# Optimization experiments

Hardware: AMD Instinct MI355X
Metric: run time of the kernel (lower is better)

The kernel has to match this reference:

```python
import jax, jax.numpy as jnp
import numpy as np
from jax import lax

DN = ('NCHW', 'OIHW', 'NCHW')
EPS = 1e-9
MASK_THR = 1e-3


def box_filter(x, size):
    # Separable box (ones) filter with SAME padding; x: [1,1,H,W]
    pad = size // 2
    kv = jnp.ones((1, 1, size, 1), x.dtype)
    kh = jnp.ones((1, 1, 1, size), x.dtype)
    y = lax.conv_general_dilated(x, kv, (1, 1), [(pad, pad), (0, 0)], dimension_numbers=DN)
    return lax.conv_general_dilated(y, kh, (1, 1), [(0, 0), (pad, pad)], dimension_numbers=DN)


def setup_inputs() -> dict:
    key = jax.random.key(0)
    k1, k2, k3, k4 = jax.random.split(key, 4)
    H = W = 2048
    I = jax.random.uniform(k1, (1, 1, H, W), jnp.float32)            # image in [0,1]
    u = jax.random.uniform(k2, (1, 4, H, W), jnp.float32)            # class memberships
    b = 1.0 + 0.1 * jax.random.normal(k3, (1, 1, H, W), jnp.float32)  # bias field ~1
    e = jax.random.normal(k4, (1, 1, H, W), jnp.float32) * 0.1       # residual
    return {"I": I, "u": u, "b": b, "e": e, "p": 2, "size": 21}


def reference(I, u, b, e, p, size):
    C = u.shape[1]
    e_d = lax.stop_gradient(e)
    b_d = lax.stop_gradient(b)
    up = u ** p                      # [1,C,H,W]
    b2 = b_d * b_d
    mask = (I > MASK_THR).astype(I.dtype)
    norm = box_filter(mask, size)    # partialFilter: local valid-pixel count

    def filt(x):                     # convParFilt: mask-normalized local mean
        return box_filter(x, size) / (norm + EPS)

    b_K = filt(b)
    b2_K = filt(b2)

    # classCenter (vectorized over classes 1..C-1)
    A = (I - e_d) * b_K                                   # [1,1,H,W]
    num = jnp.sum(A * up[:, 1:], axis=(0, 2, 3))          # [C-1]
    den = jnp.sum(b2_K * up[:, 1:], axis=(0, 2, 3))       # [C-1]
    c0 = jnp.sum(I * up[:, :1]) / (jnp.sum(up[:, :1]) + EPS)
    v = jnp.concatenate([c0[None], num / (den + EPS)])    # [C]

    # bias-field update: convolution is linear, so sum over classes first
    vb = v[None, :, None, None]
    bd = filt((I - e_d) * jnp.sum(vb * up, axis=1, keepdims=True))
    db = filt(jnp.sum(vb * vb * up, axis=1, keepdims=True))
    bd = bd * mask + (1.0 - mask)
    db = db * mask + (1.0 - mask)
    b_new = bd / (db + EPS)
    diff = b - b_new
    return jnp.mean(diff * diff)
```

## Files before the change

kernel.cpp:

```cpp
#include <hip/hip_runtime.h>

constexpr int Hh = 2048;
constexpr int Ww = 2048;
constexpr int NN = Hh * Ww;
constexpr int W4 = Ww / 4;
constexpr int NN4 = NN / 4;
constexpr int RAD = 10;
constexpr float EPSf = 1e-9f;
constexpr float MASK_THRf = 0.001f;
constexpr int SEGW = 58;
constexpr int NSEG = 9;
constexpr int BH = 8;
constexpr int NBAND = Hh / BH;
constexpr int NWAVE = NSEG * NBAND;
constexpr int WPB = 3;
constexpr int SPB = NSEG / WPB;
constexpr int NBLK = NBAND * SPB;
constexpr int NXCD = 8;
constexpr int CPX = NBLK / NXCD;

__device__ inline float rcpf(float x) { return __builtin_amdgcn_rcpf(x); }

__device__ inline float waveReduce(float v) {
    #pragma unroll
    for (int o = 32; o > 0; o >>= 1) v += __shfl_down(v, o, 64);
    return v;
}

__device__ inline float4 f4zero() { float4 z; z.x = z.y = z.z = z.w = 0.f; return z; }

__device__ inline float4 hbox(float4 v, int lane) {
    float S = v.x + v.y + v.z + v.w;
    float Sm2 = __shfl(S, lane - 2, 64);
    float Sm1 = __shfl(S, lane - 1, 64);
    float Sp1 = __shfl(S, lane + 1, 64);
    float Sp2 = __shfl(S, lane + 2, 64);
    float T5 = Sm2 + Sm1 + S + Sp1 + Sp2;
    float wm3 = __shfl(v.w, lane - 3, 64);
    float zm3 = __shfl(v.z, lane - 3, 64);
    float xm2 = __shfl(v.x, lane - 2, 64);
    float wp2 = __shfl(v.w, lane + 2, 64);
    float xp3 = __shfl(v.x, lane + 3, 64);
    float yp3 = __shfl(v.y, lane + 3, 64);
    float4 r;
    r.y = T5 + wm3;
    r.z = T5 + xp3;
    r.x = r.y + zm3 - wp2;
    r.w = r.z + yp3 - xm2;
    return r;
}

__device__ inline void winA(float4& sm, float4& sb, float4& sq,
                            float4 iv, float4 bv, float f) {
    sm.x += f * ((iv.x > MASK_THRf) ? 1.f : 0.f);
    sm.y += f * ((iv.y > MASK_THRf) ? 1.f : 0.f);
    sm.z += f * ((iv.z > MASK_THRf) ? 1.f : 0.f);
    sm.w += f * ((iv.w > MASK_THRf) ? 1.f : 0.f);
    sb.x += f * bv.x; sb.y += f * bv.y; sb.z += f * bv.z; sb.w += f * bv.w;
    sq.x += f * (bv.x * bv.x); sq.y += f * (bv.y * bv.y);
    sq.z += f * (bv.z * bv.z); sq.w += f * (bv.w * bv.w);
}

__device__ inline void winB(float4& sp, float4& sq, float4& sm,
                            float4 pv, float4 qv, float4 iv, float f) {
    sp.x += f * pv.x; sp.y += f * pv.y; sp.z += f * pv.z; sp.w += f * pv.w;
    sq.x += f * qv.x; sq.y += f * qv.y; sq.z += f * qv.z; sq.w += f * qv.w;
    sm.x += f * ((iv.x > MASK_THRf) ? 1.f : 0.f);
    sm.y += f * ((iv.y > MASK_THRf) ? 1.f : 0.f);
    sm.z += f * ((iv.z > MASK_THRf) ? 1.f : 0.f);
    sm.w += f * ((iv.w > MASK_THRf) ? 1.f : 0.f);
}

__device__ inline void k2_pix(float bm, float bb, float bb2, float Iv, float ev,
                              float u0, float u1, float u2, float u3, float* a) {
    float rn = rcpf(bm + EPSf);
    float bK = bb * rn;
    float b2K = bb2 * rn;
    float p0 = u0 * u0, p1 = u1 * u1, p2 = u2 * u2, p3 = u3 * u3;
    a[0] += Iv * p0;
    a[1] += p0;
    float A = (Iv - ev) * bK;
    a[2] += A * p1; a[3] += A * p2; a[4] += A * p3;
    a[5] += b2K * p1; a[6] += b2K * p2; a[7] += b2K * p3;
}

__device__ inline int xcdSwz(int b) { return (b % NXCD) * CPX + b / NXCD; }

__global__ __launch_bounds__(192, 2) void kA(
        const float* __restrict__ I, const float* __restrict__ B,
        const float* __restrict__ E, const float* __restrict__ U,
        float* __restrict__ partA) {
    int lane = threadIdx.x & 63;
    int wave = threadIdx.x >> 6;
    int orig = xcdSwz(blockIdx.x);
    int band = orig / SPB;
    int sb = orig - band * SPB;
    int strip = sb * WPB + wave;
    int wid = orig * WPB + wave;
    int xc = strip * SEGW - 3 + lane;
    bool inb = (unsigned)xc < (unsigned)W4;
    int xl = inb ? xc : 0;
    int y0 = band * BH;

    const float4* I4 = (const float4*)I;
    const float4* B4 = (const float4*)B;
    const float4* E4 = (const float4*)E;
    const float4* U0 = (const float4*)U;
    const float4* U1 = U0 + NN4;
    const float4* U2 = U1 + NN4;
    const float4* U3 = U2 + NN4;

    float4 sm = f4zero(), sb4 = f4zero(), sq = f4zero();
    #pragma unroll
    for (int k = 0; k < 2 * RAD + 1; ++k) {
        int r = y0 - RAD - 1 + k;
        float f = ((unsigned)r < (unsigned)Hh) ? 1.f : 0.f;
        int rc = (r < 0) ? 0 : ((r > Hh - 1) ? Hh - 1 : r);
        winA(sm, sb4, sq, I4[rc * W4 + xl], B4[rc * W4 + xl], f);
    }

    float a[8] = {0, 0, 0, 0, 0, 0, 0, 0};
    #pragma unroll 1
    for (int yy = 0; yy < BH; yy += 2) {
        int y = y0 + yy;
        int hd0 = y + RAD, hd1 = y + RAD + 1;
        int tl0 = y - RAD - 1, tl1 = y - RAD;
        float fh0 = (hd0 < Hh) ? 1.f : 0.f;
        float fh1 = (hd1 < Hh) ? 1.f : 0.f;
        float ft0 = (tl0 >= 0) ? -1.f : 0.f;
        float ft1 = (tl1 >= 0) ? -1.f : 0.f;
        int rh0 = (hd0 < Hh) ? hd0 : Hh - 1;
        int rh1 = (hd1 < Hh) ? hd1 : Hh - 1;
        int rt0 = (tl0 >= 0) ? tl0 : 0;
        int rt1 = (tl1 >= 0) ? tl1 : 0;
        float4 ih0 = I4[rh0 * W4 + xl], bh0 = B4[rh0 * W4 + xl];
        float4 ih1 = I4[rh1 * W4 + xl], bh1 = B4[rh1 * W4 + xl];
        float4 it0 = I4[rt0 * W4 + xl], bt0 = B4[rt0 * W4 + xl];
        float4 it1 = I4[rt1 * W4 + xl], bt1 = B4[rt1 * W4 + xl];
        int xo0 = y * W4 + xl, xo1 = (y + 1) * W4 + xl;
        float4 Iv0 = I4[xo0], Ev0 = E4[xo0];
        float4 u00 = U0[xo0], u10 = U1[xo0], u20 = U2[xo0], u30 = U3[xo0];
        float4 Iv1 = I4[xo1], Ev1 = E4[xo1];
        float4 u01 = U0[xo1], u11 = U1[xo1], u21 = U2[xo1], u31 = U3[xo1];
        winA(sm, sb4, sq, ih0, bh0, fh0);
        winA(sm, sb4, sq, it0, bt0, ft0);
        {
            float4 vm = inb ? sm : f4zero();
            float4 vb = inb ? sb4 : f4zero();
            float4 vq = inb ? sq : f4zero();
            float4 bm = hbox(vm, lane);
            float4 bb = hbox(vb, lane);
            float4 bq = hbox(vq, lane);
            if (inb && lane >= 3 && lane <= 60) {
                k2_pix(bm.x, bb.x, bq.x, Iv0.x, Ev0.x, u00.x, u10.x, u20.x, u30.x, a);
                k2_pix(bm.y, bb.y, bq.y, Iv0.y, Ev0.y, u00.y, u10.y, u20.y, u30.y, a);
                k2_pix(bm.z, bb.z, bq.z, Iv0.z, Ev0.z, u00.z, u10.z, u20.z, u30.z, a);
                k2_pix(bm.w, bb.w, bq.w, Iv0.w, Ev0.w, u00.w, u10.w, u20.w, u30.w, a);
            }
        }
        winA(sm, sb4, sq, ih1, bh1, fh1);
        winA(sm, sb4, sq, it1, bt1, ft1);
        {
            float4 vm = inb ? sm : f4zero();
            float4 vb = inb ? sb4 : f4zero();
            float4 vq = inb ? sq : f4zero();
            float4 bm = hbox(vm, lane);
            float4 bb = hbox(vb, lane);
            float4 bq = hbox(vq, lane);
            if (inb && lane >= 3 && lane <= 60) {
                k2_pix(bm.x, bb.x, bq.x, Iv1.x, Ev1.x, u01.x, u11.x, u21.x, u31.x, a);
                k2_pix(bm.y, bb.y, bq.y, Iv1.y, Ev1.y, u01.y, u11.y, u21.y, u31.y, a);
                k2_pix(bm.z, bb.z, bq.z, Iv1.z, Ev1.z, u01.z, u11.z, u21.z, u31.z, a);
                k2_pix(bm.w, bb.w, bq.w, Iv1.w, Ev1.w, u01.w, u11.w, u21.w, u31.w, a);
            }
        }
    }

    #pragma unroll
    for (int k = 0; k < 8; ++k) a[k] = waveReduce(a[k]);
    if (lane == 0) {
        float4 r0, r1;
        r0.x = a[0]; r0.y = a[1]; r0.z = a[2]; r0.w = a[3];
        r1.x = a[4]; r1.y = a[5]; r1.z = a[6]; r1.w = a[7];
        ((float4*)partA)[wid * 2]     = r0;
        ((float4*)partA)[wid * 2 + 1] = r1;
    }
}

__global__ __launch_bounds__(1024) void k3_v(const float* __restrict__ partA, float* __restrict__ vV) {
    __shared__ float s[1024];
    int tid = threadIdx.x;
    float acc = 0.f;
    #pragma unroll
    for (int j = 0; j < (NWAVE * 8) / 1024; ++j) acc += partA[tid + j * 1024];
    s[tid] = acc;
    __syncthreads();
    #pragma unroll
    for (int st = 512; st >= 8; st >>= 1) {
        if (tid < st) s[tid] += s[tid + st];
        __syncthreads();
    }
    if (tid == 0) {
        vV[0] = s[0] / (s[1] + EPSf);
        vV[1] = s[2] / (s[5] + EPSf);
        vV[2] = s[3] / (s[6] + EPSf);
        vV[3] = s[4] / (s[7] + EPSf);
    }
}

__global__ __launch_bounds__(256) void kP(
        const float* __restrict__ I, const float* __restrict__ E, const float* __restrict__ U,
        const float* __restrict__ vV,
        float* __restrict__ P, float* __restrict__ Q) {
    int idx = blockIdx.x * 256 + threadIdx.x;
    float v0 = vV[0], v1 = vV[1], v2 = vV[2], v3 = vV[3];
    float w0 = v0 * v0, w1 = v1 * v1, w2 = v2 * v2, w3 = v3 * v3;
    const float4* I4 = (const float4*)I;
    const float4* E4 = (const float4*)E;
    const float4* U0 = (const float4*)U;
    const float4* U1 = U0 + NN4;
    const float4* U2 = U1 + NN4;
    const float4* U3 = U2 + NN4;
    float4 Iv = I4[idx], Ev = E4[idx];
    float4 a0 = U0[idx], a1 = U1[idx], a2 = U2[idx], a3 = U3[idx];
    float4 p, q;
    float p0, p1, p2, p3;
    p0 = a0.x * a0.x; p1 = a1.x * a1.x; p2 = a2.x * a2.x; p3 = a3.x * a3.x;
    p.x = (Iv.x - Ev.x) * (v0 * p0 + v1 * p1 + v2 * p2 + v3 * p3);
    q.x = w0 * p0 + w1 * p1 + w2 * p2 + w3 * p3;
    p0 = a0.y * a0.y; p1 = a1.y * a1.y; p2 = a2.y * a2.y; p3 = a3.y * a3.y;
    p.y = (Iv.y - Ev.y) * (v0 * p0 + v1 * p1 + v2 * p2 + v3 * p3);
    q.y = w0 * p0 + w1 * p1 + w2 * p2 + w3 * p3;
    p0 = a0.z * a0.z; p1 = a1.z * a1.z; p2 = a2.z * a2.z; p3 = a3.z * a3.z;
    p.z = (Iv.z - Ev.z) * (v0 * p0 + v1 * p1 + v2 * p2 + v3 * p3);
    q.z = w0 * p0 + w1 * p1 + w2 * p2 + w3 * p3;
    p0 = a0.w * a0.w; p1 = a1.w * a1.w; p2 = a2.w * a2.w; p3 = a3.w * a3.w;
    p.w = (Iv.w - Ev.w) * (v0 * p0 + v1 * p1 + v2 * p2 + v3 * p3);
    q.w = w0 * p0 + w1 * p1 + w2 * p2 + w3 * p3;
    ((float4*)P)[idx] = p;
    ((float4*)Q)[idx] = q;
}

__global__ __launch_bounds__(192, 2) void kB(
        const float* __restrict__ P, const float* __restrict__ Q,
        const float* __restrict__ I, const float* __restrict__ B,
        float* __restrict__ partL) {
    int lane = threadIdx.x & 63;
    int wave = threadIdx.x >> 6;
    int orig = xcdSwz(blockIdx.x);
    int band = orig / SPB;
    int sb = orig - band * SPB;
    int strip = sb * WPB + wave;
    int wid = orig * WPB + wave;
    int xc = strip * SEGW - 3 + lane;
    bool inb = (unsigned)xc < (unsigned)W4;
    int xl = inb ? xc : 0;
    int y0 = band * BH;

    const float4* P4 = (const float4*)P;
    const float4* Q4 = (const float4*)Q;
    const float4* I4 = (const float4*)I;
    const float4* B4 = (const float4*)B;

    float4 sp = f4zero(), sqq = f4zero(), sm = f4zero();
    #pragma unroll
    for (int k = 0; k < 2 * RAD + 1; ++k) {
        int r = y0 - RAD - 1 + k;
        float f = ((unsigned)r < (unsigned)Hh) ? 1.f : 0.f;
        int rc = (r < 0) ? 0 : ((r > Hh - 1) ? Hh - 1 : r);
        winB(sp, sqq, sm, P4[rc * W4 + xl], Q4[rc * W4 + xl], I4[rc * W4 + xl], f);
    }

    float a = 0.f;
    #pragma unroll 1
    for (int yy = 0; yy < BH; yy += 2) {
        int y = y0 + yy;
        int hd0 = y + RAD, hd1 = y + RAD + 1;
        int tl0 = y - RAD - 1, tl1 = y - RAD;
        float fh0 = (hd0 < Hh) ? 1.f : 0.f;
        float fh1 = (hd1 < Hh) ? 1.f : 0.f;
        float ft0 = (tl0 >= 0) ? -1.f : 0.f;
        float ft1 = (tl1 >= 0) ? -1.f : 0.f;
        int rh0 = (hd0 < Hh) ? hd0 : Hh - 1;
        int rh1 = (hd1 < Hh) ? hd1 : Hh - 1;
        int rt0 = (tl0 >= 0) ? tl0 : 0;
        int rt1 = (tl1 >= 0) ? tl1 : 0;
        float4 ph0 = P4[rh0 * W4 + xl], qh0 = Q4[rh0 * W4 + xl], mh0 = I4[rh0 * W4 + xl];
        float4 ph1 = P4[rh1 * W4 + xl], qh1 = Q4[rh1 * W4 + xl], mh1 = I4[rh1 * W4 + xl];
        float4 pt0 = P4[rt0 * W4 + xl], qt0 = Q4[rt0 * W4 + xl], mt0 = I4[rt0 * W4 + xl];
        float4 pt1 = P4[rt1 * W4 + xl], qt1 = Q4[rt1 * W4 + xl], mt1 = I4[rt1 * W4 + xl];
        int xo0 = y * W4 + xl, xo1 = (y + 1) * W4 + xl;
        float4 Iv0 = I4[xo0], Bv0 = B4[xo0];
        float4 Iv1 = I4[xo1], Bv1 = B4[xo1];
        winB(sp, sqq, sm, ph0, qh0, mh0, fh0);
        winB(sp, sqq, sm, pt0, qt0, mt0, ft0);
        {
            float4 vP = inb ? sp : f4zero();
            float4 vQ = inb ? sqq : f4zero();
            float4 vM = inb ? sm : f4zero();
            float4 bP = hbox(vP, lane);
            float4 bQ = hbox(vQ, lane);
            float4 bM = hbox(vM, lane);
            if (inb && lane >= 3 && lane <= 60) {
                {
                    float rn = rcpf(bM.x + EPSf);
                    float bd = bP.x * rn, db = bQ.x * rn;
                    float m = (Iv0.x > MASK_THRf) ? 1.f : 0.f;
                    bd = bd * m + (1.f - m); db = db * m + (1.f - m);
                    float d = Bv0.x - bd * rcpf(db + EPSf); a += d * d;
                }
                {
                    float rn = rcpf(bM.y + EPSf);
                    float bd = bP.y * rn, db = bQ.y * rn;
                    float m = (Iv0.y > MASK_THRf) ? 1.f : 0.f;
                    bd = bd * m + (1.f - m); db = db * m + (1.f - m);
                    float d = Bv0.y - bd * rcpf(db + EPSf); a += d * d;
                }
                {
                    float rn = rcpf(bM.z + EPSf);
                    float bd = bP.z * rn, db = bQ.z * rn;
                    float m = (Iv0.z > MASK_THRf) ? 1.f : 0.f;
                    bd = bd * m + (1.f - m); db = db * m + (1.f - m);
                    float d = Bv0.z - bd * rcpf(db + EPSf); a += d * d;
                }
                {
                    float rn = rcpf(bM.w + EPSf);
                    float bd = bP.w * rn, db = bQ.w * rn;
                    float m = (Iv0.w > MASK_THRf) ? 1.f : 0.f;
                    bd = bd * m + (1.f - m); db = db * m + (1.f - m);
                    float d = Bv0.w - bd * rcpf(db + EPSf); a += d * d;
                }
            }
        }
        winB(sp, sqq, sm, ph1, qh1, mh1, fh1);
        winB(sp, sqq, sm, pt1, qt1, mt1, ft1);
        {
            float4 vP = inb ? sp : f4zero();
            float4 vQ = inb ? sqq : f4zero();
            float4 vM = inb ? sm : f4zero();
            float4 bP = hbox(vP, lane);
            float4 bQ = hbox(vQ, lane);
            float4 bM = hbox(vM, lane);
            if (inb && lane >= 3 && lane <= 60) {
                {
                    float rn = rcpf(bM.x + EPSf);
                    float bd = bP.x * rn, db = bQ.x * rn;
                    float m = (Iv1.x > MASK_THRf) ? 1.f : 0.f;
                    bd = bd * m + (1.f - m); db = db * m + (1.f - m);
                    float d = Bv1.x - bd * rcpf(db + EPSf); a += d * d;
                }
                {
                    float rn = rcpf(bM.y + EPSf);
                    float bd = bP.y * rn, db = bQ.y * rn;
                    float m = (Iv1.y > MASK_THRf) ? 1.f : 0.f;
                    bd = bd * m + (1.f - m); db = db * m + (1.f - m);
                    float d = Bv1.y - bd * rcpf(db + EPSf); a += d * d;
                }
                {
                    float rn = rcpf(bM.z + EPSf);
                    float bd = bP.z * rn, db = bQ.z * rn;
                    float m = (Iv1.z > MASK_THRf) ? 1.f : 0.f;
                    bd = bd * m + (1.f - m); db = db * m + (1.f - m);
                    float d = Bv1.z - bd * rcpf(db + EPSf); a += d * d;
                }
                {
                    float rn = rcpf(bM.w + EPSf);
                    float bd = bP.w * rn, db = bQ.w * rn;
                    float m = (Iv1.w > MASK_THRf) ? 1.f : 0.f;
                    bd = bd * m + (1.f - m); db = db * m + (1.f - m);
                    float d = Bv1.w - bd * rcpf(db + EPSf); a += d * d;
                }
            }
        }
    }

    a = waveReduce(a);
    if (lane == 0) partL[wid] = a;
}

__global__ __launch_bounds__(1024) void k6_out(const float* __restrict__ partL, float* __restrict__ out) {
    __shared__ float s[1024];
    int tid = threadIdx.x;
    float acc = 0.f;
    for (int c = tid; c < NWAVE; c += 1024) acc += partL[c];
    s[tid] = acc;
    __syncthreads();
    #pragma unroll
    for (int st = 512; st >= 1; st >>= 1) {
        if (tid < st) s[tid] += s[tid + st];
        __syncthreads();
    }
    if (tid == 0) out[0] = s[0] / (float)NN;
}

extern "C" void kernel_launch(void* const* d_in, const int* in_sizes, int n_in,
                              void* d_out, int out_size, void* d_ws, size_t ws_size,
                              hipStream_t stream) {
    const float* I = (const float*)d_in[0];
    const float* U = (const float*)d_in[1];
    const float* B = (const float*)d_in[2];
    const float* E = (const float*)d_in[3];

    float* P     = (float*)d_ws;
    float* Q     = P + NN;
    float* partA = Q + NN;
    float* partL = partA + NWAVE * 8;
    float* vV    = partL + NWAVE;

    kA<<<NBLK, 192, 0, stream>>>(I, B, E, U, partA);
    k3_v<<<1, 1024, 0, stream>>>(partA, vV);
    kP<<<NN4 / 256, 256, 0, stream>>>(I, E, U, vV, P, Q);
    kB<<<NBLK, 192, 0, stream>>>(P, Q, I, B, partL);
    k6_out<<<1, 1024, 0, stream>>>(partL, (float*)d_out);
}
```

Measured before the change: 199.6 us.

## Fuse P/Q computation into sliding-window kernel and drop intermediate buffers

Removes the separate kP kernel that wrote the P and Q planes to workspace. kB now recomputes P and Q on the fly from I, E and the four U planes for every row entering or leaving the vertical window. This trades a 32 MB write plus reread for reading six input planes per window update, about twice as many loads per row, plus redundant ALU work. Launch bounds for kA and kB also change from 2 to 3 blocks per SIMD, which tightens the register budget and may cause spills.

```diff
diff --git a/kernel.cpp b/kernel.cpp
--- a/kernel.cpp
+++ b/kernel.cpp
@@ -84,9 +84,29 @@
     a[5] += b2K * p1; a[6] += b2K * p2; a[7] += b2K * p3;
 }
 
+__device__ inline void pqCalc(float4 iv, float4 ev,
+                              float4 a0, float4 a1, float4 a2, float4 a3,
+                              float v0, float v1, float v2, float v3,
+                              float w0, float w1, float w2, float w3,
+                              float4& pv, float4& qv) {
+    float p0, p1, p2, p3;
+    p0 = a0.x * a0.x; p1 = a1.x * a1.x; p2 = a2.x * a2.x; p3 = a3.x * a3.x;
+    pv.x = (iv.x - ev.x) * (v0 * p0 + v1 * p1 + v2 * p2 + v3 * p3);
+    qv.x = w0 * p0 + w1 * p1 + w2 * p2 + w3 * p3;
+    p0 = a0.y * a0.y; p1 = a1.y * a1.y; p2 = a2.y * a2.y; p3 = a3.y * a3.y;
+    pv.y = (iv.y - ev.y) * (v0 * p0 + v1 * p1 + v2 * p2 + v3 * p3);
+    qv.y = w0 * p0 + w1 * p1 + w2 * p2 + w3 * p3;
+    p0 = a0.z * a0.z; p1 = a1.z * a1.z; p2 = a2.z * a2.z; p3 = a3.z * a3.z;
+    pv.z = (iv.z - ev.z) * (v0 * p0 + v1 * p1 + v2 * p2 + v3 * p3);
+    qv.z = w0 * p0 + w1 * p1 + w2 * p2 + w3 * p3;
+    p0 = a0.w * a0.w; p1 = a1.w * a1.w; p2 = a2.w * a2.w; p3 = a3.w * a3.w;
+    pv.w = (iv.w - ev.w) * (v0 * p0 + v1 * p1 + v2 * p2 + v3 * p3);
+    qv.w = w0 * p0 + w1 * p1 + w2 * p2 + w3 * p3;
+}
+
 __device__ inline int xcdSwz(int b) { return (b % NXCD) * CPX + b / NXCD; }
 
-__global__ __launch_bounds__(192, 2) void kA(
+__global__ __launch_bounds__(192, 3) void kA(
         const float* __restrict__ I, const float* __restrict__ B,
         const float* __restrict__ E, const float* __restrict__ U,
         float* __restrict__ partA) {
@@ -208,42 +228,10 @@
     }
 }
 
-__global__ __launch_bounds__(256) void kP(
-        const float* __restrict__ I, const float* __restrict__ E, const float* __restrict__ U,
+__global__ __launch_bounds__(192, 3) void kB(
+        const float* __restrict__ I, const float* __restrict__ E,
+        const float* __restrict__ U, const float* __restrict__ B,
         const float* __restrict__ vV,
-        float* __restrict__ P, float* __restrict__ Q) {
-    int idx = blockIdx.x * 256 + threadIdx.x;
-    float v0 = vV[0], v1 = vV[1], v2 = vV[2], v3 = vV[3];
-    float w0 = v0 * v0, w1 = v1 * v1, w2 = v2 * v2, w3 = v3 * v3;
-    const float4* I4 = (const float4*)I;
-    const float4* E4 = (const float4*)E;
-    const float4* U0 = (const float4*)U;
-    const float4* U1 = U0 + NN4;
-    const float4* U2 = U1 + NN4;
-    const float4* U3 = U2 + NN4;
-    float4 Iv = I4[idx], Ev = E4[idx];
-    float4 a0 = U0[idx], a1 = U1[idx], a2 = U2[idx], a3 = U3[idx];
-    float4 p, q;
-    float p0, p1, p2, p3;
-    p0 = a0.x * a0.x; p1 = a1.x * a1.x; p2 = a2.x * a2.x; p3 = a3.x * a3.x;
-    p.x = (Iv.x - Ev.x) * (v0 * p0 + v1 * p1 + v2 * p2 + v3 * p3);
-    q.x = w0 * p0 + w1 * p1 + w2 * p2 + w3 * p3;
-    p0 = a0.y * a0.y; p1 = a1.y * a1.y; p2 = a2.y * a2.y; p3 = a3.y * a3.y;
-    p.y = (Iv.y - Ev.y) * (v0 * p0 + v1 * p1 + v2 * p2 + v3 * p3);
-    q.y = w0 * p0 + w1 * p1 + w2 * p2 + w3 * p3;
-    p0 = a0.z * a0.z; p1 = a1.z * a1.z; p2 = a2.z * a2.z; p3 = a3.z * a3.z;
-    p.z = (Iv.z - Ev.z) * (v0 * p0 + v1 * p1 + v2 * p2 + v3 * p3);
-    q.z = w0 * p0 + w1 * p1 + w2 * p2 + w3 * p3;
-    p0 = a0.w * a0.w; p1 = a1.w * a1.w; p2 = a2.w * a2.w; p3 = a3.w * a3.w;
-    p.w = (Iv.w - Ev.w) * (v0 * p0 + v1 * p1 + v2 * p2 + v3 * p3);
-    q.w = w0 * p0 + w1 * p1 + w2 * p2 + w3 * p3;
-    ((float4*)P)[idx] = p;
-    ((float4*)Q)[idx] = q;
-}
-
-__global__ __launch_bounds__(192, 2) void kB(
-        const float* __restrict__ P, const float* __restrict__ Q,
-        const float* __restrict__ I, const float* __restrict__ B,
         float* __restrict__ partL) {
     int lane = threadIdx.x & 63;
     int wave = threadIdx.x >> 6;
@@ -257,18 +245,29 @@
     int xl = inb ? xc : 0;
     int y0 = band * BH;
 
-    const float4* P4 = (const float4*)P;
-    const float4* Q4 = (const float4*)Q;
     const float4* I4 = (const float4*)I;
+    const float4* E4 = (const float4*)E;
     const float4* B4 = (const float4*)B;
+    const float4* U0 = (const float4*)U;
+    const float4* U1 = U0 + NN4;
+    const float4* U2 = U1 + NN4;
+    const float4* U3 = U2 + NN4;
+
+    float v0 = vV[0], v1 = vV[1], v2 = vV[2], v3 = vV[3];
+    float w0 = v0 * v0, w1 = v1 * v1, w2 = v2 * v2, w3 = v3 * v3;
 
     float4 sp = f4zero(), sqq = f4zero(), sm = f4zero();
-    #pragma unroll
+    #pragma unroll 1
     for (int k = 0; k < 2 * RAD + 1; ++k) {
         int r = y0 - RAD - 1 + k;
         float f = ((unsigned)r < (unsigned)Hh) ? 1.f : 0.f;
         int rc = (r < 0) ? 0 : ((r > Hh - 1) ? Hh - 1 : r);
-        winB(sp, sqq, sm, P4[rc * W4 + xl], Q4[rc * W4 + xl], I4[rc * W4 + xl], f);
+        int xo = rc * W4 + xl;
+        float4 iv = I4[xo], ev = E4[xo];
+        float4 a0 = U0[xo], a1 = U1[xo], a2 = U2[xo], a3 = U3[xo];
+        float4 pv, qv;
+        pqCalc(iv, ev, a0, a1, a2, a3, v0, v1, v2, v3, w0, w1, w2, w3, pv, qv);
+        winB(sp, sqq, sm, pv, qv, iv, f);
     }
 
     float a = 0.f;
@@ -285,15 +284,26 @@
         int rh1 = (hd1 < Hh) ? hd1 : Hh - 1;
         int rt0 = (tl0 >= 0) ? tl0 : 0;
         int rt1 = (tl1 >= 0) ? tl1 : 0;
-        float4 ph0 = P4[rh0 * W4 + xl], qh0 = Q4[rh0 * W4 + xl], mh0 = I4[rh0 * W4 + xl];
-        float4 ph1 = P4[rh1 * W4 + xl], qh1 = Q4[rh1 * W4 + xl], mh1 = I4[rh1 * W4 + xl];
-        float4 pt0 = P4[rt0 * W4 + xl], qt0 = Q4[rt0 * W4 + xl], mt0 = I4[rt0 * W4 + xl];
-        float4 pt1 = P4[rt1 * W4 + xl], qt1 = Q4[rt1 * W4 + xl], mt1 = I4[rt1 * W4 + xl];
+        int xh0 = rh0 * W4 + xl, xh1 = rh1 * W4 + xl;
+        int xt0 = rt0 * W4 + xl, xt1 = rt1 * W4 + xl;
+        float4 ih0 = I4[xh0], eh0 = E4[xh0];
+        float4 ah00 = U0[xh0], ah10 = U1[xh0], ah20 = U2[xh0], ah30 = U3[xh0];
+        float4 ih1 = I4[xh1], eh1 = E4[xh1];
+        float4 ah01 = U0[xh1], ah11 = U1[xh1], ah21 = U2[xh1], ah31 = U3[xh1];
+        float4 it0 = I4[xt0], et0 = E4[xt0];
+        float4 at00 = U0[xt0], at10 = U1[xt0], at20 = U2[xt0], at30 = U3[xt0];
+        float4 it1 = I4[xt1], et1 = E4[xt1];
+        float4 at01 = U0[xt1], at11 = U1[xt1], at21 = U2[xt1], at31 = U3[xt1];
         int xo0 = y * W4 + xl, xo1 = (y + 1) * W4 + xl;
         float4 Iv0 = I4[xo0], Bv0 = B4[xo0];
         float4 Iv1 = I4[xo1], Bv1 = B4[xo1];
-        winB(sp, sqq, sm, ph0, qh0, mh0, fh0);
-        winB(sp, sqq, sm, pt0, qt0, mt0, ft0);
+        {
+            float4 pv, qv;
+            pqCalc(ih0, eh0, ah00, ah10, ah20, ah30, v0, v1, v2, v3, w0, w1, w2, w3, pv, qv);
+            winB(sp, sqq, sm, pv, qv, ih0, fh0);
+            pqCalc(it0, et0, at00, at10, at20, at30, v0, v1, v2, v3, w0, w1, w2, w3, pv, qv);
+            winB(sp, sqq, sm, pv, qv, it0, ft0);
+        }
         {
             float4 vP = inb ? sp : f4zero();
             float4 vQ = inb ? sqq : f4zero();
@@ -332,8 +342,13 @@
                 }
             }
         }
-        winB(sp, sqq, sm, ph1, qh1, mh1, fh1);
-        winB(sp, sqq, sm, pt1, qt1, mt1, ft1);
+        {
+            float4 pv, qv;
+            pqCalc(ih1, eh1, ah01, ah11, ah21, ah31, v0, v1, v2, v3, w0, w1, w2, w3, pv, qv);
+            winB(sp, sqq, sm, pv, qv, ih1, fh1);
+            pqCalc(it1, et1, at01, at11, at21, at31, v0, v1, v2, v3, w0, w1, w2, w3, pv, qv);
+            winB(sp, sqq, sm, pv, qv, it1, ft1);
+        }
         {
             float4 vP = inb ? sp : f4zero();
             float4 vQ = inb ? sqq : f4zero();
@@ -401,15 +416,12 @@
     const float* B = (const float*)d_in[2];
     const float* E = (const float*)d_in[3];
 
-    float* P     = (float*)d_ws;
-    float* Q     = P + NN;
-    float* partA = Q + NN;
+    float* partA = (float*)d_ws;
     float* partL = partA + NWAVE * 8;
     float* vV    = partL + NWAVE;
 
     kA<<<NBLK, 192, 0, stream>>>(I, B, E, U, partA);
     k3_v<<<1, 1024, 0, stream>>>(partA, vV);
-    kP<<<NN4 / 256, 256, 0, stream>>>(I, E, U, vV, P, Q);
-    kB<<<NBLK, 192, 0, stream>>>(P, Q, I, B, partL);
+    kB<<<NBLK, 192, 0, stream>>>(I, E, U, B, vV, partL);
     k6_out<<<1, 1024, 0, stream>>>(partL, (float*)d_out);
 }
```

Result: slower. 225.4 us (+12.9%).
